# Performance work log

Measured on AMD Instinct MI355X. Metric: run time of the kernel, lower is better.

## Reference

```python
import jax, jax.numpy as jnp
import numpy as np

B, C, H, W = 64, 512, 32, 32   # batch, channels (=in_dim=model_dim), spatial
N, A = 1, 16                   # n_routers (forced to 1 by the view/matmul shape algebra), num_adapters
EPS = 1e-5                     # torch BatchNorm2d / LayerNorm default eps
INIT_SCALE = 0.02              # config.router_init_scale


def setup_inputs() -> dict:
    key = jax.random.key(0)
    k1, k2 = jax.random.split(key)
    x = jax.random.normal(k1, (B, C, H, W), dtype=jnp.float32)
    router_weights = jax.random.normal(k2, (N, C, A), dtype=jnp.float32) * INIT_SCALE
    router_bias = jnp.zeros((N, A), dtype=jnp.float32)
    bn_gamma = jnp.ones((N, C), dtype=jnp.float32)          # BatchNorm2d weight per router
    bn_beta = jnp.zeros((N, C), dtype=jnp.float32)          # BatchNorm2d bias per router
    ln_gamma = jnp.ones((N, C), dtype=jnp.float32) * INIT_SCALE  # LayerNorm weight (init'd to router_init_scale)
    ln_beta = jnp.zeros((N, C), dtype=jnp.float32)          # LayerNorm bias per router
    return dict(x=x, router_weights=router_weights, router_bias=router_bias,
                bn_gamma=bn_gamma, bn_beta=bn_beta, ln_gamma=ln_gamma, ln_beta=ln_beta)


def reference(x, router_weights, router_bias, bn_gamma, bn_beta, ln_gamma, ln_beta):
    # --- per-router BatchNorm2d (training-mode batch stats over N,H,W) + spatial mean pool ---
    mu = jnp.mean(x, axis=(0, 2, 3))                         # [C]
    var = jnp.var(x, axis=(0, 2, 3))                         # biased, as torch uses for normalization
    xn = (x - mu[None, :, None, None]) * jax.lax.rsqrt(var + EPS)[None, :, None, None]

    def bn_pool(g, b):  # g,b: [C] -> pooled [B,C]
        return jnp.mean(xn * g[None, :, None, None] + b[None, :, None, None], axis=(2, 3))

    new_x = jax.vmap(bn_pool)(bn_gamma, bn_beta)             # [N,B,C]

    # --- normalize_router_weights: LayerNorm over in_dim of router_weights[i].T ---
    wt = jnp.swapaxes(router_weights, 1, 2)                  # [N,A,C]
    m = jnp.mean(wt, axis=-1, keepdims=True)
    v = jnp.var(wt, axis=-1, keepdims=True)
    wn = (wt - m) * jax.lax.rsqrt(v + EPS) * ln_gamma[:, None, :] + ln_beta[:, None, :]
    wn = jnp.swapaxes(wn, 1, 2)                              # [N,C,A]

    # --- routing matmul + bias + softmax (equiv. to view(B,-1) @ W for N=1) ---
    adapter_logits = jnp.einsum('nbc,nca->nba', new_x, wn) + router_bias[:, None, :]  # [N,B,A]
    adapter_probs = jax.nn.softmax(adapter_logits, axis=-1)
    return new_x, adapter_logits, adapter_probs
```

## Files before the change

### kernel.cpp

```cpp
#include <hip/hip_runtime.h>

#define B_DIM 64
#define C_DIM 512
#define A_DIM 16
#define HW    1024
#define EPS   1e-5f

__global__ __launch_bounds__(256) void reduce_rows(const float* __restrict__ x,
                                                   float* __restrict__ s1,
                                                   float* __restrict__ sq) {
    const int bc = blockIdx.x;
    const float4* p = reinterpret_cast<const float4*>(x + (size_t)bc * HW);
    float4 v = p[threadIdx.x];
    float s = v.x + v.y + v.z + v.w;
    float q = v.x * v.x + v.y * v.y + v.z * v.z + v.w * v.w;
#pragma unroll
    for (int off = 32; off > 0; off >>= 1) {
        s += __shfl_down(s, off);
        q += __shfl_down(q, off);
    }
    __shared__ float ls[4], lq[4];
    const int wid = threadIdx.x >> 6;
    const int lane = threadIdx.x & 63;
    if (lane == 0) { ls[wid] = s; lq[wid] = q; }
    __syncthreads();
    if (threadIdx.x == 0) {
        s = ls[0] + ls[1] + ls[2] + ls[3];
        q = lq[0] + lq[1] + lq[2] + lq[3];
        const int b = bc >> 9;
        const int c = bc & (C_DIM - 1);
        s1[c * B_DIM + b] = s;
        sq[c * B_DIM + b] = q;
    }
}

__global__ __launch_bounds__(64) void stats_newx_ln(
    const float* __restrict__ s1, const float* __restrict__ sq,
    const float* __restrict__ bn_g, const float* __restrict__ bn_b,
    const float* __restrict__ rw, const float* __restrict__ ln_g,
    const float* __restrict__ ln_b,
    float* __restrict__ newx, float* __restrict__ wn_t) {
    const int lane = threadIdx.x;
    if (blockIdx.x < C_DIM) {
        const int c = blockIdx.x;
        const float s = s1[c * B_DIM + lane];
        const float q = sq[c * B_DIM + lane];
        float ts = s, tq = q;
#pragma unroll
        for (int off = 32; off > 0; off >>= 1) {
            ts += __shfl_down(ts, off);
            tq += __shfl_down(tq, off);
        }
        const float mu  = __shfl(ts, 0) * (1.0f / 65536.0f);
        const float var = __shfl(tq, 0) * (1.0f / 65536.0f) - mu * mu;
        const float r   = rsqrtf(var + EPS);
        const float nx  = bn_g[c] * (s * (1.0f / 1024.0f) - mu) * r + bn_b[c];
        newx[lane * C_DIM + c] = nx;
    } else {
        const int a = blockIdx.x - C_DIM;
        float wv[8];
        float s = 0.f, q = 0.f;
#pragma unroll
        for (int j = 0; j < 8; j++) {
            const int c = j * 64 + lane;
            wv[j] = rw[c * A_DIM + a];
            s += wv[j];
            q += wv[j] * wv[j];
        }
#pragma unroll
        for (int off = 32; off > 0; off >>= 1) {
            s += __shfl_down(s, off);
            q += __shfl_down(q, off);
        }
        const float m = __shfl(s, 0) * (1.0f / 512.0f);
        const float v = __shfl(q, 0) * (1.0f / 512.0f) - m * m;
        const float r = rsqrtf(v + EPS);
#pragma unroll
        for (int j = 0; j < 8; j++) {
            const int c = j * 64 + lane;
            wn_t[c * A_DIM + a] = (wv[j] - m) * r * ln_g[c] + ln_b[c];
        }
    }
}

__global__ __launch_bounds__(64) void matmul_softmax(
    const float* __restrict__ newx, const float* __restrict__ wn_t,
    const float* __restrict__ rbias,
    float* __restrict__ logits, float* __restrict__ probs) {
    const int b = blockIdx.x;
    const int lane = threadIdx.x;
    const int a = lane & 15;
    const int chunk = lane >> 4;
    const float* xr = newx + b * C_DIM + chunk * 128;
    const float* wr = wn_t + (chunk * 128) * A_DIM + a;
    float acc = 0.f;
#pragma unroll 8
    for (int i = 0; i < 128; i++) {
        acc += xr[i] * wr[i * A_DIM];
    }
    acc += __shfl_xor(acc, 16);
    acc += __shfl_xor(acc, 32);
    const float logit = acc + rbias[a];
    float mx = logit;
#pragma unroll
    for (int m = 1; m < 16; m <<= 1) mx = fmaxf(mx, __shfl_xor(mx, m));
    const float e = expf(logit - mx);
    float se = e;
#pragma unroll
    for (int m = 1; m < 16; m <<= 1) se += __shfl_xor(se, m);
    const float prob = e / se;
    if (lane < 16) {
        logits[b * A_DIM + lane] = logit;
        probs[b * A_DIM + lane] = prob;
    }
}

extern "C" void kernel_launch(void* const* d_in, const int* in_sizes, int n_in,
                              void* d_out, int out_size, void* d_ws, size_t ws_size,
                              hipStream_t stream) {
    const float* x     = (const float*)d_in[0];
    const float* rw    = (const float*)d_in[1];
    const float* rbias = (const float*)d_in[2];
    const float* bn_g  = (const float*)d_in[3];
    const float* bn_b  = (const float*)d_in[4];
    const float* ln_g  = (const float*)d_in[5];
    const float* ln_b  = (const float*)d_in[6];

    float* out    = (float*)d_out;
    float* newx   = out;
    float* logits = out + B_DIM * C_DIM;
    float* probs  = logits + B_DIM * A_DIM;

    float* s1   = (float*)d_ws;
    float* sq   = s1 + B_DIM * C_DIM;
    float* wn_t = sq + B_DIM * C_DIM;

    reduce_rows<<<B_DIM * C_DIM, 256, 0, stream>>>(x, s1, sq);
    stats_newx_ln<<<C_DIM + A_DIM, 64, 0, stream>>>(s1, sq, bn_g, bn_b, rw,
                                                    ln_g, ln_b, newx, wn_t);
    matmul_softmax<<<B_DIM, 64, 0, stream>>>(newx, wn_t, rbias, logits, probs);
}
```

Before: 201.9 us.

## Fuse three router kernels into one cooperative persistent kernel with grid syncs

Result: slower. 432.1 us (+114.0%).

```diff
diff --git a/kernel.cpp b/kernel.cpp
--- a/kernel.cpp
+++ b/kernel.cpp
@@ -1,4 +1,7 @@
 #include <hip/hip_runtime.h>
+#include <hip/hip_cooperative_groups.h>
+
+namespace cg = cooperative_groups;
 
 #define B_DIM 64
 #define C_DIM 512
@@ -6,43 +9,57 @@
 #define HW    1024
 #define EPS   1e-5f
 
-__global__ __launch_bounds__(256) void reduce_rows(const float* __restrict__ x,
-                                                   float* __restrict__ s1,
-                                                   float* __restrict__ sq) {
-    const int bc = blockIdx.x;
-    const float4* p = reinterpret_cast<const float4*>(x + (size_t)bc * HW);
-    float4 v = p[threadIdx.x];
-    float s = v.x + v.y + v.z + v.w;
-    float q = v.x * v.x + v.y * v.y + v.z * v.z + v.w * v.w;
+#define NBLK       1024
+#define WAVES_PB   4
+#define NWAVE      (NBLK * WAVES_PB)
+#define ROWS_PER_WAVE ((B_DIM * C_DIM) / NWAVE)
+
+__global__ __launch_bounds__(256, 4) void fused_router(
+    const float* __restrict__ x,
+    const float* __restrict__ rw,
+    const float* __restrict__ rbias,
+    const float* __restrict__ bn_g,
+    const float* __restrict__ bn_b,
+    const float* __restrict__ ln_g,
+    const float* __restrict__ ln_b,
+    float* __restrict__ newx,
+    float* __restrict__ logits,
+    float* __restrict__ probs,
+    float* __restrict__ s1,
+    float* __restrict__ sq,
+    float* __restrict__ wn_t)
+{
+    const int lane = threadIdx.x & 63;
+    const int gw   = blockIdx.x * WAVES_PB + (threadIdx.x >> 6);
+
 #pragma unroll
-    for (int off = 32; off > 0; off >>= 1) {
-        s += __shfl_down(s, off);
-        q += __shfl_down(q, off);
+    for (int i = 0; i < ROWS_PER_WAVE; ++i) {
+        const int row = gw * ROWS_PER_WAVE + i;
+        const float4* p = reinterpret_cast<const float4*>(x + (size_t)row * HW);
+        float s = 0.f, q = 0.f;
+#pragma unroll
+        for (int j = 0; j < 4; ++j) {
+            const float4 v = p[lane + 64 * j];
+            s += v.x + v.y + v.z + v.w;
+            q += v.x * v.x + v.y * v.y + v.z * v.z + v.w * v.w;
+        }
+#pragma unroll
+        for (int off = 32; off > 0; off >>= 1) {
+            s += __shfl_down(s, off);
+            q += __shfl_down(q, off);
+        }
+        if (lane == 0) {
+            const int b = row >> 9;
+            const int c = row & (C_DIM - 1);
+            s1[c * B_DIM + b] = s;
+            sq[c * B_DIM + b] = q;
+        }
     }
-    __shared__ float ls[4], lq[4];
-    const int wid = threadIdx.x >> 6;
-    const int lane = threadIdx.x & 63;
-    if (lane == 0) { ls[wid] = s; lq[wid] = q; }
-    __syncthreads();
-    if (threadIdx.x == 0) {
-        s = ls[0] + ls[1] + ls[2] + ls[3];
-        q = lq[0] + lq[1] + lq[2] + lq[3];
-        const int b = bc >> 9;
-        const int c = bc & (C_DIM - 1);
-        s1[c * B_DIM + b] = s;
-        sq[c * B_DIM + b] = q;
-    }
-}
 
-__global__ __launch_bounds__(64) void stats_newx_ln(
-    const float* __restrict__ s1, const float* __restrict__ sq,
-    const float* __restrict__ bn_g, const float* __restrict__ bn_b,
-    const float* __restrict__ rw, const float* __restrict__ ln_g,
-    const float* __restrict__ ln_b,
-    float* __restrict__ newx, float* __restrict__ wn_t) {
-    const int lane = threadIdx.x;
-    if (blockIdx.x < C_DIM) {
-        const int c = blockIdx.x;
+    cg::this_grid().sync();
+
+    if (gw < C_DIM) {
+        const int c = gw;
         const float s = s1[c * B_DIM + lane];
         const float q = sq[c * B_DIM + lane];
         float ts = s, tq = q;
@@ -54,16 +71,14 @@
         const float mu  = __shfl(ts, 0) * (1.0f / 65536.0f);
         const float var = __shfl(tq, 0) * (1.0f / 65536.0f) - mu * mu;
         const float r   = rsqrtf(var + EPS);
-        const float nx  = bn_g[c] * (s * (1.0f / 1024.0f) - mu) * r + bn_b[c];
-        newx[lane * C_DIM + c] = nx;
-    } else {
-        const int a = blockIdx.x - C_DIM;
+        newx[lane * C_DIM + c] = bn_g[c] * (s * (1.0f / 1024.0f) - mu) * r + bn_b[c];
+    } else if (gw < C_DIM + A_DIM) {
+        const int a = gw - C_DIM;
         float wv[8];
         float s = 0.f, q = 0.f;
 #pragma unroll
-        for (int j = 0; j < 8; j++) {
-            const int c = j * 64 + lane;
-            wv[j] = rw[c * A_DIM + a];
+        for (int j = 0; j < 8; ++j) {
+            wv[j] = rw[(j * 64 + lane) * A_DIM + a];
             s += wv[j];
             q += wv[j] * wv[j];
         }
@@ -76,42 +91,39 @@
         const float v = __shfl(q, 0) * (1.0f / 512.0f) - m * m;
         const float r = rsqrtf(v + EPS);
 #pragma unroll
-        for (int j = 0; j < 8; j++) {
+        for (int j = 0; j < 8; ++j) {
             const int c = j * 64 + lane;
             wn_t[c * A_DIM + a] = (wv[j] - m) * r * ln_g[c] + ln_b[c];
         }
     }
-}
 
-__global__ __launch_bounds__(64) void matmul_softmax(
-    const float* __restrict__ newx, const float* __restrict__ wn_t,
-    const float* __restrict__ rbias,
-    float* __restrict__ logits, float* __restrict__ probs) {
-    const int b = blockIdx.x;
-    const int lane = threadIdx.x;
-    const int a = lane & 15;
-    const int chunk = lane >> 4;
-    const float* xr = newx + b * C_DIM + chunk * 128;
-    const float* wr = wn_t + (chunk * 128) * A_DIM + a;
-    float acc = 0.f;
+    cg::this_grid().sync();
+
+    if (gw < B_DIM) {
+        const int b = gw;
+        const int a = lane & 15;
+        const int chunk = lane >> 4;
+        const float* xr = newx + b * C_DIM + chunk * 128;
+        const float* wr = wn_t + (chunk * 128) * A_DIM + a;
+        float acc = 0.f;
 #pragma unroll 8
-    for (int i = 0; i < 128; i++) {
-        acc += xr[i] * wr[i * A_DIM];
-    }
-    acc += __shfl_xor(acc, 16);
-    acc += __shfl_xor(acc, 32);
-    const float logit = acc + rbias[a];
-    float mx = logit;
+        for (int i = 0; i < 128; i++) {
+            acc += xr[i] * wr[i * A_DIM];
+        }
+        acc += __shfl_xor(acc, 16);
+        acc += __shfl_xor(acc, 32);
+        const float logit = acc + rbias[a];
+        float mx = logit;
 #pragma unroll
-    for (int m = 1; m < 16; m <<= 1) mx = fmaxf(mx, __shfl_xor(mx, m));
-    const float e = expf(logit - mx);
-    float se = e;
+        for (int m = 1; m < 16; m <<= 1) mx = fmaxf(mx, __shfl_xor(mx, m));
+        const float e = expf(logit - mx);
+        float se = e;
 #pragma unroll
-    for (int m = 1; m < 16; m <<= 1) se += __shfl_xor(se, m);
-    const float prob = e / se;
-    if (lane < 16) {
-        logits[b * A_DIM + lane] = logit;
-        probs[b * A_DIM + lane] = prob;
+        for (int m = 1; m < 16; m <<= 1) se += __shfl_xor(se, m);
+        if (lane < 16) {
+            logits[b * A_DIM + lane] = logit;
+            probs[b * A_DIM + lane] = e / se;
+        }
     }
 }
 
@@ -135,8 +147,11 @@
     float* sq   = s1 + B_DIM * C_DIM;
     float* wn_t = sq + B_DIM * C_DIM;
 
-    reduce_rows<<<B_DIM * C_DIM, 256, 0, stream>>>(x, s1, sq);
-    stats_newx_ln<<<C_DIM + A_DIM, 64, 0, stream>>>(s1, sq, bn_g, bn_b, rw,
-                                                    ln_g, ln_b, newx, wn_t);
-    matmul_softmax<<<B_DIM, 64, 0, stream>>>(newx, wn_t, rbias, logits, probs);
+    void* args[] = { (void*)&x, (void*)&rw, (void*)&rbias, (void*)&bn_g,
+                     (void*)&bn_b, (void*)&ln_g, (void*)&ln_b,
+                     (void*)&newx, (void*)&logits, (void*)&probs,
+                     (void*)&s1, (void*)&sq, (void*)&wn_t };
+
+    hipLaunchCooperativeKernel((const void*)fused_router, dim3(NBLK), dim3(256),
+                               args, 0, stream);
 }
```
